# Kernel tuning notes

Measured on AMD Instinct MI355X. Metric: run time of the kernel, lower is better.

The kernel has to match this reference:

```python
import jax, jax.numpy as jnp
import numpy as np

NEG_INF = -1e9  # stand-in for -inf so fully-masked rows stay finite


def setup_inputs() -> dict:
    key = jax.random.key(0)
    ks = jax.random.split(key, 7)
    B, Nq, Nkv, H, D = 8, 512, 512, 16, 256
    return {
        "v_inv": jax.random.normal(ks[0], (B, Nkv, D), dtype=jnp.float32),
        "messages": jax.random.normal(ks[1], (B, Nq, Nkv, H), dtype=jnp.float32),
        "adj_matrix": jax.random.randint(ks[2], (B, Nq, Nkv), 0, 2, dtype=jnp.int32),
        "W_in": jax.random.normal(ks[3], (D, D), dtype=jnp.float32) * (1.0 / np.sqrt(D)),
        "b_in": jax.random.normal(ks[4], (D,), dtype=jnp.float32) * 0.02,
        "W_out": jax.random.normal(ks[5], (D, D), dtype=jnp.float32) * (1.0 / np.sqrt(D)),
        "b_out": jax.random.normal(ks[6], (D,), dtype=jnp.float32) * 0.02,
    }


def reference(v_inv, messages, adj_matrix, W_in, b_in, W_out, b_out):
    H = messages.shape[-1]
    D = v_inv.shape[-1]
    d_head = D // H
    # adjacency -> additive attention mask (0 where edge, -inf where not)
    attn_mask = jnp.where(adj_matrix > 0, 0.0, NEG_INF).astype(messages.dtype)
    logits = messages + attn_mask[..., None]          # [B, Nq, Nkv, H]
    attn = jax.nn.softmax(logits, axis=2)             # softmax over N_kv
    # value projection and head split
    proj = v_inv @ W_in.T + b_in                      # [B, Nkv, D]
    head_feats = proj.reshape(*proj.shape[:-1], H, d_head)  # [B, Nkv, H, dh]
    # per-head weighted aggregation of value features
    attn_out = jnp.einsum("bqkh,bkhd->bqhd", attn, head_feats)  # [B, Nq, H, dh]
    # L2 norm of attention row per head, used as a rescale
    weights = jnp.sqrt(jnp.sum(attn * attn, axis=2))  # [B, Nq, H]
    attn_out = attn_out * weights[..., None]
    attn_out = attn_out.reshape(*attn_out.shape[:-2], D)  # [B, Nq, D]
    return attn_out @ W_out.T + b_out
```

## Files before the change

### kernel.cpp

```cpp
#include <hip/hip_runtime.h>

constexpr int NQ = 512;
constexpr int NKV = 512;
constexpr int Hh = 16;
constexpr int Dd = 256;

__global__ __launch_bounds__(256) void gemm_bias(
    const float* __restrict__ A, const float* __restrict__ W,
    const float* __restrict__ bias, float* __restrict__ C) {
  __shared__ float As[64][68];
  __shared__ float Ws[64][68];
  const int t = threadIdx.x;
  const int tx = t & 15, ty = t >> 4;
  const int m0 = blockIdx.x * 64, n0 = blockIdx.y * 64;

  float acc[4][4] = {};
  float4 av[4], wv[4];

#pragma unroll
  for (int i = 0; i < 4; ++i) {
    const int flat = i * 256 + t;
    const int r = flat >> 4, c4 = (flat & 15) << 2;
    av[i] = *(const float4*)(A + (size_t)(m0 + r) * 256 + c4);
    wv[i] = *(const float4*)(W + (size_t)(n0 + r) * 256 + c4);
  }

  for (int kb = 0; kb < 4; ++kb) {
#pragma unroll
    for (int i = 0; i < 4; ++i) {
      const int flat = i * 256 + t;
      const int r = flat >> 4, c4 = (flat & 15) << 2;
      As[c4 + 0][r] = av[i].x; As[c4 + 1][r] = av[i].y;
      As[c4 + 2][r] = av[i].z; As[c4 + 3][r] = av[i].w;
      Ws[c4 + 0][r] = wv[i].x; Ws[c4 + 1][r] = wv[i].y;
      Ws[c4 + 2][r] = wv[i].z; Ws[c4 + 3][r] = wv[i].w;
    }
    __syncthreads();
    if (kb < 3) {
#pragma unroll
      for (int i = 0; i < 4; ++i) {
        const int flat = i * 256 + t;
        const int r = flat >> 4, c4 = (flat & 15) << 2;
        av[i] = *(const float4*)(A + (size_t)(m0 + r) * 256 + (kb + 1) * 64 + c4);
        wv[i] = *(const float4*)(W + (size_t)(n0 + r) * 256 + (kb + 1) * 64 + c4);
      }
    }
#pragma unroll 16
    for (int k = 0; k < 64; ++k) {
      float a_[4], w_[4];
      *(float4*)a_ = *(const float4*)&As[k][ty << 2];
      *(float4*)w_ = *(const float4*)&Ws[k][tx << 2];
#pragma unroll
      for (int i = 0; i < 4; ++i)
#pragma unroll
        for (int j = 0; j < 4; ++j)
          acc[i][j] = fmaf(a_[i], w_[j], acc[i][j]);
    }
    if (kb < 3) __syncthreads();
  }

  const float4 bv = *(const float4*)(bias + n0 + (tx << 2));
  const float bb[4] = {bv.x, bv.y, bv.z, bv.w};
#pragma unroll
  for (int i = 0; i < 4; ++i) {
    float4 cv;
    cv.x = acc[i][0] + bb[0]; cv.y = acc[i][1] + bb[1];
    cv.z = acc[i][2] + bb[2]; cv.w = acc[i][3] + bb[3];
    *(float4*)(C + (size_t)(m0 + (ty << 2) + i) * 256 + n0 + (tx << 2)) = cv;
  }
}

__global__ __launch_bounds__(512) void attn_fused(
    const float* __restrict__ msg, const int* __restrict__ adj,
    const float* __restrict__ proj, float* __restrict__ attn_out) {
  __shared__ float Esh[2][4][4][16][20];

  const int t    = threadIdx.x;
  const int lane = t & 63;
  const int w    = t >> 6;
  const int oct  = w >> 1;
  const int qh   = w & 1;
  const int h    = lane >> 2;
  const int d4   = lane & 3;
  const int col  = lane << 2;
  const int q0   = blockIdx.x * 4;
  const int b    = blockIdx.y;

  const int p_h4  = t & 3;
  const int p_q   = (t >> 2) & 3;
  const int p_oct = (t >> 4) & 3;
  const int p_kp  = t >> 6;

  const float* mrow  = msg + ((size_t)(b * NQ + q0 + p_q) * NKV) * Hh + p_h4 * 4;
  const int*   arow  = adj + (size_t)(b * NQ + q0 + p_q) * NKV;
  const float* pbase = proj + (size_t)b * NKV * Dd;

  float4 o0 = {}, o1 = {};
  float s0 = 0.f, s1 = 0.f, r0 = 0.f, r1 = 0.f;

  float4 mv0, mv1;
  int2 aa;

  const int ql0 = qh * 2, ql1 = qh * 2 + 1;
  const int eh0 = h ^ ql0, eh1 = h ^ ql1;

  {
    const int kg = p_oct * 128 + p_kp * 2;
    mv0 = *(const float4*)(mrow + (size_t)kg * Hh);
    mv1 = *(const float4*)(mrow + (size_t)(kg + 1) * Hh);
    aa = *(const int2*)(arow + kg);
    float e0[4], e1[4];
    e0[0] = aa.x > 0 ? __expf(mv0.x) : 0.f; e0[1] = aa.x > 0 ? __expf(mv0.y) : 0.f;
    e0[2] = aa.x > 0 ? __expf(mv0.z) : 0.f; e0[3] = aa.x > 0 ? __expf(mv0.w) : 0.f;
    e1[0] = aa.y > 0 ? __expf(mv1.x) : 0.f; e1[1] = aa.y > 0 ? __expf(mv1.y) : 0.f;
    e1[2] = aa.y > 0 ? __expf(mv1.z) : 0.f; e1[3] = aa.y > 0 ? __expf(mv1.w) : 0.f;
#pragma unroll
    for (int i = 0; i < 4; ++i) {
      const int h2 = (p_h4 * 4 + i) ^ p_q;
      *(float2*)&Esh[0][p_oct][p_q][h2][p_kp * 2] = make_float2(e0[i], e1[i]);
    }
  }
  __syncthreads();

#pragma unroll 1
  for (int rd = 0; rd < 8; ++rd) {
    const int cur = rd & 1, nxt = cur ^ 1;
    if (rd < 7) {
      const int kg = p_oct * 128 + (rd + 1) * 16 + p_kp * 2;
      mv0 = *(const float4*)(mrow + (size_t)kg * Hh);
      mv1 = *(const float4*)(mrow + (size_t)(kg + 1) * Hh);
      aa = *(const int2*)(arow + kg);
    }

    __builtin_amdgcn_s_setprio(1);
#pragma unroll 1
    for (int kq = 0; kq < 4; ++kq) {
      const float* prow =
          pbase + (size_t)(oct * 128 + rd * 16 + kq * 4) * Dd + col;
      const float4 p0 = *(const float4*)(prow);
      const float4 p1 = *(const float4*)(prow + Dd);
      const float4 p2 = *(const float4*)(prow + 2 * Dd);
      const float4 p3 = *(const float4*)(prow + 3 * Dd);
      const float4 ea = *(const float4*)&Esh[cur][oct][ql0][eh0][kq * 4];
      const float4 eb = *(const float4*)&Esh[cur][oct][ql1][eh1][kq * 4];
      s0 += ea.x + ea.y + ea.z + ea.w;
      r0 = fmaf(ea.x, ea.x, fmaf(ea.y, ea.y,
           fmaf(ea.z, ea.z, fmaf(ea.w, ea.w, r0))));
      o0.x = fmaf(ea.x, p0.x, o0.x); o0.y = fmaf(ea.x, p0.y, o0.y);
      o0.z = fmaf(ea.x, p0.z, o0.z); o0.w = fmaf(ea.x, p0.w, o0.w);
      o0.x = fmaf(ea.y, p1.x, o0.x); o0.y = fmaf(ea.y, p1.y, o0.y);
      o0.z = fmaf(ea.y, p1.z, o0.z); o0.w = fmaf(ea.y, p1.w, o0.w);
      o0.x = fmaf(ea.z, p2.x, o0.x); o0.y = fmaf(ea.z, p2.y, o0.y);
      o0.z = fmaf(ea.z, p2.z, o0.z); o0.w = fmaf(ea.z, p2.w, o0.w);
      o0.x = fmaf(ea.w, p3.x, o0.x); o0.y = fmaf(ea.w, p3.y, o0.y);
      o0.z = fmaf(ea.w, p3.z, o0.z); o0.w = fmaf(ea.w, p3.w, o0.w);
      s1 += eb.x + eb.y + eb.z + eb.w;
      r1 = fmaf(eb.x, eb.x, fmaf(eb.y, eb.y,
           fmaf(eb.z, eb.z, fmaf(eb.w, eb.w, r1))));
      o1.x = fmaf(eb.x, p0.x, o1.x); o1.y = fmaf(eb.x, p0.y, o1.y);
      o1.z = fmaf(eb.x, p0.z, o1.z); o1.w = fmaf(eb.x, p0.w, o1.w);
      o1.x = fmaf(eb.y, p1.x, o1.x); o1.y = fmaf(eb.y, p1.y, o1.y);
      o1.z = fmaf(eb.y, p1.z, o1.z); o1.w = fmaf(eb.y, p1.w, o1.w);
      o1.x = fmaf(eb.z, p2.x, o1.x); o1.y = fmaf(eb.z, p2.y, o1.y);
      o1.z = fmaf(eb.z, p2.z, o1.z); o1.w = fmaf(eb.z, p2.w, o1.w);
      o1.x = fmaf(eb.w, p3.x, o1.x); o1.y = fmaf(eb.w, p3.y, o1.y);
      o1.z = fmaf(eb.w, p3.z, o1.z); o1.w = fmaf(eb.w, p3.w, o1.w);
    }
    __builtin_amdgcn_s_setprio(0);

    if (rd < 7) {
      float e0[4], e1[4];
      e0[0] = aa.x > 0 ? __expf(mv0.x) : 0.f; e0[1] = aa.x > 0 ? __expf(mv0.y) : 0.f;
      e0[2] = aa.x > 0 ? __expf(mv0.z) : 0.f; e0[3] = aa.x > 0 ? __expf(mv0.w) : 0.f;
      e1[0] = aa.y > 0 ? __expf(mv1.x) : 0.f; e1[1] = aa.y > 0 ? __expf(mv1.y) : 0.f;
      e1[2] = aa.y > 0 ? __expf(mv1.z) : 0.f; e1[3] = aa.y > 0 ? __expf(mv1.w) : 0.f;
#pragma unroll
      for (int i = 0; i < 4; ++i) {
        const int h2 = (p_h4 * 4 + i) ^ p_q;
        *(float2*)&Esh[nxt][p_oct][p_q][h2][p_kp * 2] = make_float2(e0[i], e1[i]);
      }
    }
    __syncthreads();
  }

  float* base = &Esh[0][0][0][0][0];
  float4* Ro = (float4*)base;
  float*  Rs = base + 2048;
  float*  Rr = base + 2176;

  __syncthreads();
  if (w >= 4) {
    const int reg = w - 4;
    Ro[(reg * 2 + 0) * 64 + lane] = o0;
    Ro[(reg * 2 + 1) * 64 + lane] = o1;
    if (d4 == 0) {
      Rs[(reg * 2 + 0) * 16 + h] = s0; Rs[(reg * 2 + 1) * 16 + h] = s1;
      Rr[(reg * 2 + 0) * 16 + h] = r0; Rr[(reg * 2 + 1) * 16 + h] = r1;
    }
  }
  __syncthreads();
  if (w < 4) {
    const float4 v0 = Ro[(w * 2 + 0) * 64 + lane];
    const float4 v1 = Ro[(w * 2 + 1) * 64 + lane];
    o0.x += v0.x; o0.y += v0.y; o0.z += v0.z; o0.w += v0.w;
    o1.x += v1.x; o1.y += v1.y; o1.z += v1.z; o1.w += v1.w;
    s0 += Rs[(w * 2 + 0) * 16 + h]; s1 += Rs[(w * 2 + 1) * 16 + h];
    r0 += Rr[(w * 2 + 0) * 16 + h]; r1 += Rr[(w * 2 + 1) * 16 + h];
  }
  __syncthreads();
  if (w == 2 || w == 3) {
    const int reg = w - 2;
    Ro[(reg * 2 + 0) * 64 + lane] = o0;
    Ro[(reg * 2 + 1) * 64 + lane] = o1;
    if (d4 == 0) {
      Rs[(reg * 2 + 0) * 16 + h] = s0; Rs[(reg * 2 + 1) * 16 + h] = s1;
      Rr[(reg * 2 + 0) * 16 + h] = r0; Rr[(reg * 2 + 1) * 16 + h] = r1;
    }
  }
  __syncthreads();
  if (w < 2) {
    const float4 v0 = Ro[(w * 2 + 0) * 64 + lane];
    const float4 v1 = Ro[(w * 2 + 1) * 64 + lane];
    o0.x += v0.x; o0.y += v0.y; o0.z += v0.z; o0.w += v0.w;
    o1.x += v1.x; o1.y += v1.y; o1.z += v1.z; o1.w += v1.w;
    const float st0 = s0 + Rs[(w * 2 + 0) * 16 + h];
    const float st1 = s1 + Rs[(w * 2 + 1) * 16 + h];
    const float rt0 = r0 + Rr[(w * 2 + 0) * 16 + h];
    const float rt1 = r1 + Rr[(w * 2 + 1) * 16 + h];
    const float wg0 = sqrtf(rt0) / (st0 * st0);
    const float wg1 = sqrtf(rt1) / (st1 * st1);
    float4 u0, u1;
    u0.x = o0.x * wg0; u0.y = o0.y * wg0; u0.z = o0.z * wg0; u0.w = o0.w * wg0;
    u1.x = o1.x * wg1; u1.y = o1.y * wg1; u1.z = o1.z * wg1; u1.w = o1.w * wg1;
    *(float4*)(attn_out + (size_t)(b * NQ + q0 + w * 2 + 0) * Dd + col) = u0;
    *(float4*)(attn_out + (size_t)(b * NQ + q0 + w * 2 + 1) * Dd + col) = u1;
  }
}

extern "C" void kernel_launch(void* const* d_in, const int* in_sizes, int n_in,
                              void* d_out, int out_size, void* d_ws, size_t ws_size,
                              hipStream_t stream) {
  const float* v_inv    = (const float*)d_in[0];
  const float* messages = (const float*)d_in[1];
  const int*   adj      = (const int*)d_in[2];
  const float* W_in     = (const float*)d_in[3];
  const float* b_in     = (const float*)d_in[4];
  const float* W_out    = (const float*)d_in[5];
  const float* b_out    = (const float*)d_in[6];
  float* out = (float*)d_out;

  float* proj = (float*)d_ws;
  float* attn = proj + (size_t)8 * NKV * Dd;

  dim3 gg(64, 4);
  gemm_bias<<<gg, 256, 0, stream>>>(v_inv, W_in, b_in, proj);
  attn_fused<<<dim3(128, 8), 512, 0, stream>>>(messages, adj, proj, attn);
  gemm_bias<<<gg, 256, 0, stream>>>(attn, W_out, b_out, out);
}
```

Baseline: 266.5 us.

## Shrink attention blocks to 2 queries and 256 threads with staggered KV octants

The fused attention kernel now gives each block 2 queries instead of 4 and 256 threads instead of 512, which doubles the grid. Each wave owns one KV octant, rotated by block index so concurrent blocks read different parts of proj. The exp staging buffer and the cross-wave reduction shrink to match, and the KV loop takes 16 rounds of 8 keys. This is meant to raise occupancy and spread L2 traffic, but each proj row is now reused by only 2 queries, so proj reads double and there are more barriers per key.

```diff
diff --git a/kernel.cpp b/kernel.cpp
--- a/kernel.cpp
+++ b/kernel.cpp
@@ -70,26 +70,26 @@
   }
 }
 
-__global__ __launch_bounds__(512) void attn_fused(
+__global__ __launch_bounds__(256) void attn_fused(
     const float* __restrict__ msg, const int* __restrict__ adj,
     const float* __restrict__ proj, float* __restrict__ attn_out) {
-  __shared__ float Esh[2][4][4][16][20];
+  __shared__ float Esh[2][4][2][16][10];
 
   const int t    = threadIdx.x;
   const int lane = t & 63;
   const int w    = t >> 6;
-  const int oct  = w >> 1;
-  const int qh   = w & 1;
+  const int bx   = blockIdx.x;
+  const int oct  = (w + bx) & 3;
   const int h    = lane >> 2;
   const int d4   = lane & 3;
   const int col  = lane << 2;
-  const int q0   = blockIdx.x * 4;
+  const int q0   = bx * 2;
   const int b    = blockIdx.y;
 
   const int p_h4  = t & 3;
-  const int p_q   = (t >> 2) & 3;
-  const int p_oct = (t >> 4) & 3;
-  const int p_kp  = t >> 6;
+  const int p_q   = (t >> 2) & 1;
+  const int p_oct = (t >> 3) & 3;
+  const int p_k   = t >> 5;
 
   const float* mrow  = msg + ((size_t)(b * NQ + q0 + p_q) * NKV) * Hh + p_h4 * 4;
   const int*   arow  = adj + (size_t)(b * NQ + q0 + p_q) * NKV;
@@ -98,51 +98,44 @@
   float4 o0 = {}, o1 = {};
   float s0 = 0.f, s1 = 0.f, r0 = 0.f, r1 = 0.f;
 
-  float4 mv0, mv1;
-  int2 aa;
-
-  const int ql0 = qh * 2, ql1 = qh * 2 + 1;
-  const int eh0 = h ^ ql0, eh1 = h ^ ql1;
+  float4 mv;
+  int aa;
 
   {
-    const int kg = p_oct * 128 + p_kp * 2;
-    mv0 = *(const float4*)(mrow + (size_t)kg * Hh);
-    mv1 = *(const float4*)(mrow + (size_t)(kg + 1) * Hh);
-    aa = *(const int2*)(arow + kg);
-    float e0[4], e1[4];
-    e0[0] = aa.x > 0 ? __expf(mv0.x) : 0.f; e0[1] = aa.x > 0 ? __expf(mv0.y) : 0.f;
-    e0[2] = aa.x > 0 ? __expf(mv0.z) : 0.f; e0[3] = aa.x > 0 ? __expf(mv0.w) : 0.f;
-    e1[0] = aa.y > 0 ? __expf(mv1.x) : 0.f; e1[1] = aa.y > 0 ? __expf(mv1.y) : 0.f;
-    e1[2] = aa.y > 0 ? __expf(mv1.z) : 0.f; e1[3] = aa.y > 0 ? __expf(mv1.w) : 0.f;
-#pragma unroll
-    for (int i = 0; i < 4; ++i) {
-      const int h2 = (p_h4 * 4 + i) ^ p_q;
-      *(float2*)&Esh[0][p_oct][p_q][h2][p_kp * 2] = make_float2(e0[i], e1[i]);
-    }
+    const int kg = p_oct * 128 + p_k;
+    mv = *(const float4*)(mrow + (size_t)kg * Hh);
+    aa = arow[kg];
+    float e[4];
+    e[0] = aa > 0 ? __expf(mv.x) : 0.f;
+    e[1] = aa > 0 ? __expf(mv.y) : 0.f;
+    e[2] = aa > 0 ? __expf(mv.z) : 0.f;
+    e[3] = aa > 0 ? __expf(mv.w) : 0.f;
+#pragma unroll
+    for (int i = 0; i < 4; ++i)
+      Esh[0][p_oct][p_q][(p_h4 * 4 + i) ^ p_q][p_k] = e[i];
   }
   __syncthreads();
 
 #pragma unroll 1
-  for (int rd = 0; rd < 8; ++rd) {
+  for (int rd = 0; rd < 16; ++rd) {
     const int cur = rd & 1, nxt = cur ^ 1;
-    if (rd < 7) {
-      const int kg = p_oct * 128 + (rd + 1) * 16 + p_kp * 2;
-      mv0 = *(const float4*)(mrow + (size_t)kg * Hh);
-      mv1 = *(const float4*)(mrow + (size_t)(kg + 1) * Hh);
-      aa = *(const int2*)(arow + kg);
+    if (rd < 15) {
+      const int kg = p_oct * 128 + (rd + 1) * 8 + p_k;
+      mv = *(const float4*)(mrow + (size_t)kg * Hh);
+      aa = arow[kg];
     }
 
     __builtin_amdgcn_s_setprio(1);
 #pragma unroll 1
-    for (int kq = 0; kq < 4; ++kq) {
+    for (int kq = 0; kq < 2; ++kq) {
       const float* prow =
-          pbase + (size_t)(oct * 128 + rd * 16 + kq * 4) * Dd + col;
+          pbase + (size_t)(oct * 128 + rd * 8 + kq * 4) * Dd + col;
       const float4 p0 = *(const float4*)(prow);
       const float4 p1 = *(const float4*)(prow + Dd);
       const float4 p2 = *(const float4*)(prow + 2 * Dd);
       const float4 p3 = *(const float4*)(prow + 3 * Dd);
-      const float4 ea = *(const float4*)&Esh[cur][oct][ql0][eh0][kq * 4];
-      const float4 eb = *(const float4*)&Esh[cur][oct][ql1][eh1][kq * 4];
+      const float4 ea = *(const float4*)&Esh[cur][oct][0][h][kq * 4];
+      const float4 eb = *(const float4*)&Esh[cur][oct][1][h ^ 1][kq * 4];
       s0 += ea.x + ea.y + ea.z + ea.w;
       r0 = fmaf(ea.x, ea.x, fmaf(ea.y, ea.y,
            fmaf(ea.z, ea.z, fmaf(ea.w, ea.w, r0))));
@@ -168,29 +161,27 @@
     }
     __builtin_amdgcn_s_setprio(0);
 
-    if (rd < 7) {
-      float e0[4], e1[4];
-      e0[0] = aa.x > 0 ? __expf(mv0.x) : 0.f; e0[1] = aa.x > 0 ? __expf(mv0.y) : 0.f;
-      e0[2] = aa.x > 0 ? __expf(mv0.z) : 0.f; e0[3] = aa.x > 0 ? __expf(mv0.w) : 0.f;
-      e1[0] = aa.y > 0 ? __expf(mv1.x) : 0.f; e1[1] = aa.y > 0 ? __expf(mv1.y) : 0.f;
-      e1[2] = aa.y > 0 ? __expf(mv1.z) : 0.f; e1[3] = aa.y > 0 ? __expf(mv1.w) : 0.f;
-#pragma unroll
-      for (int i = 0; i < 4; ++i) {
-        const int h2 = (p_h4 * 4 + i) ^ p_q;
-        *(float2*)&Esh[nxt][p_oct][p_q][h2][p_kp * 2] = make_float2(e0[i], e1[i]);
-      }
+    if (rd < 15) {
+      float e[4];
+      e[0] = aa > 0 ? __expf(mv.x) : 0.f;
+      e[1] = aa > 0 ? __expf(mv.y) : 0.f;
+      e[2] = aa > 0 ? __expf(mv.z) : 0.f;
+      e[3] = aa > 0 ? __expf(mv.w) : 0.f;
+#pragma unroll
+      for (int i = 0; i < 4; ++i)
+        Esh[nxt][p_oct][p_q][(p_h4 * 4 + i) ^ p_q][p_k] = e[i];
     }
     __syncthreads();
   }
 
   float* base = &Esh[0][0][0][0][0];
   float4* Ro = (float4*)base;
-  float*  Rs = base + 2048;
-  float*  Rr = base + 2176;
-
-  __syncthreads();
-  if (w >= 4) {
-    const int reg = w - 4;
+  float*  Rs = base + 1024;
+  float*  Rr = base + 1088;
+
+  __syncthreads();
+  if (w >= 2) {
+    const int reg = w - 2;
     Ro[(reg * 2 + 0) * 64 + lane] = o0;
     Ro[(reg * 2 + 1) * 64 + lane] = o1;
     if (d4 == 0) {
@@ -199,7 +190,7 @@
     }
   }
   __syncthreads();
-  if (w < 4) {
+  if (w < 2) {
     const float4 v0 = Ro[(w * 2 + 0) * 64 + lane];
     const float4 v1 = Ro[(w * 2 + 1) * 64 + lane];
     o0.x += v0.x; o0.y += v0.y; o0.z += v0.z; o0.w += v0.w;
@@ -208,32 +199,31 @@
     r0 += Rr[(w * 2 + 0) * 16 + h]; r1 += Rr[(w * 2 + 1) * 16 + h];
   }
   __syncthreads();
-  if (w == 2 || w == 3) {
-    const int reg = w - 2;
-    Ro[(reg * 2 + 0) * 64 + lane] = o0;
-    Ro[(reg * 2 + 1) * 64 + lane] = o1;
+  if (w == 1) {
+    Ro[0 * 64 + lane] = o0;
+    Ro[1 * 64 + lane] = o1;
     if (d4 == 0) {
-      Rs[(reg * 2 + 0) * 16 + h] = s0; Rs[(reg * 2 + 1) * 16 + h] = s1;
-      Rr[(reg * 2 + 0) * 16 + h] = r0; Rr[(reg * 2 + 1) * 16 + h] = r1;
-    }
-  }
-  __syncthreads();
-  if (w < 2) {
-    const float4 v0 = Ro[(w * 2 + 0) * 64 + lane];
-    const float4 v1 = Ro[(w * 2 + 1) * 64 + lane];
+      Rs[0 * 16 + h] = s0; Rs[1 * 16 + h] = s1;
+      Rr[0 * 16 + h] = r0; Rr[1 * 16 + h] = r1;
+    }
+  }
+  __syncthreads();
+  if (w == 0) {
+    const float4 v0 = Ro[0 * 64 + lane];
+    const float4 v1 = Ro[1 * 64 + lane];
     o0.x += v0.x; o0.y += v0.y; o0.z += v0.z; o0.w += v0.w;
     o1.x += v1.x; o1.y += v1.y; o1.z += v1.z; o1.w += v1.w;
-    const float st0 = s0 + Rs[(w * 2 + 0) * 16 + h];
-    const float st1 = s1 + Rs[(w * 2 + 1) * 16 + h];
-    const float rt0 = r0 + Rr[(w * 2 + 0) * 16 + h];
-    const float rt1 = r1 + Rr[(w * 2 + 1) * 16 + h];
+    const float st0 = s0 + Rs[0 * 16 + h];
+    const float st1 = s1 + Rs[1 * 16 + h];
+    const float rt0 = r0 + Rr[0 * 16 + h];
+    const float rt1 = r1 + Rr[1 * 16 + h];
     const float wg0 = sqrtf(rt0) / (st0 * st0);
     const float wg1 = sqrtf(rt1) / (st1 * st1);
     float4 u0, u1;
     u0.x = o0.x * wg0; u0.y = o0.y * wg0; u0.z = o0.z * wg0; u0.w = o0.w * wg0;
     u1.x = o1.x * wg1; u1.y = o1.y * wg1; u1.z = o1.z * wg1; u1.w = o1.w * wg1;
-    *(float4*)(attn_out + (size_t)(b * NQ + q0 + w * 2 + 0) * Dd + col) = u0;
-    *(float4*)(attn_out + (size_t)(b * NQ + q0 + w * 2 + 1) * Dd + col) = u1;
+    *(float4*)(attn_out + (size_t)(b * NQ + q0 + 0) * Dd + col) = u0;
+    *(float4*)(attn_out + (size_t)(b * NQ + q0 + 1) * Dd + col) = u1;
   }
 }
 
@@ -254,6 +244,6 @@
 
   dim3 gg(64, 4);
   gemm_bias<<<gg, 256, 0, stream>>>(v_inv, W_in, b_in, proj);
-  attn_fused<<<dim3(128, 8), 512, 0, stream>>>(messages, adj, proj, attn);
+  attn_fused<<<dim3(256, 8), 256, 0, stream>>>(messages, adj, proj, attn);
   gemm_bias<<<gg, 256, 0, stream>>>(attn, W_out, b_out, out);
 }
```

After: 287.1 us. 7.7% more time.
